# Kernel optimization log

Measured on AMD Instinct MI355X. Metric: run time of the kernel, lower is better.

## Reference

```python
import jax, jax.numpy as jnp
import numpy as np

N, E, F_IN, H, L = 100000, 1600000, 256, 128, 4
ALPHA, THETA, EPS = 0.1, 0.5, 1e-5


def setup_inputs() -> dict:
    key = jax.random.key(0)
    ks = jax.random.split(key, 6)
    x = jax.random.normal(ks[0], (N, F_IN), dtype=jnp.float32)
    edge_index = jax.random.randint(ks[1], (2, E), 0, N, dtype=jnp.int32)
    lin0_w = jax.random.normal(ks[2], (F_IN, H), dtype=jnp.float32) / np.sqrt(F_IN)
    lin0_b = jnp.zeros((H,), dtype=jnp.float32)
    conv_w = jax.random.normal(ks[3], (L, H, H), dtype=jnp.float32) / np.sqrt(H)
    bn_gamma = jnp.ones((L - 1, H), dtype=jnp.float32)
    bn_beta = jnp.zeros((L - 1, H), dtype=jnp.float32)
    return {"x": x, "edge_index": edge_index, "lin0_w": lin0_w, "lin0_b": lin0_b,
            "conv_w": conv_w, "bn_gamma": bn_gamma, "bn_beta": bn_beta}


def reference(x, edge_index, lin0_w, lin0_b, conv_w, bn_gamma, bn_beta):
    n = x.shape[0]
    loops = jnp.arange(n, dtype=edge_index.dtype)
    row = jnp.concatenate([edge_index[0], loops])  # source
    col = jnp.concatenate([edge_index[1], loops])  # target
    # GCN symmetric normalization with self-loops: D^{-1/2}(A+I)D^{-1/2}
    deg = jax.ops.segment_sum(jnp.ones_like(col, dtype=x.dtype), col, num_segments=n)
    dinv = jnp.where(deg > 0, jax.lax.rsqrt(deg), 0.0)
    norm = (dinv[row] * dinv[col])[:, None]  # [E+N, 1]

    def prop(h):  # sparse aggregation: out[c] += norm * h[r]
        return jax.ops.segment_sum(h[row] * norm, col, num_segments=n)

    # GCNConv input layer
    z = prop(x @ lin0_w) + lin0_b
    x0 = z
    for i in range(L):
        h = prop(z)
        beta = float(np.log(THETA / (i + 1) + 1.0))
        s = (1.0 - ALPHA) * h + ALPHA * x0          # identity mapping to initial features
        z = (1.0 - beta) * s + beta * (s @ conv_w[i])  # shared_weights GCN2Conv
        if i < L - 1:
            mu = jnp.mean(z, axis=0)
            var = jnp.mean((z - mu) ** 2, axis=0)
            z = (z - mu) * jax.lax.rsqrt(var + EPS) * bn_gamma[i] + bn_beta[i]
            z = jax.nn.relu(z)
    return z
```

## Files before the change

### kernel.cpp

```cpp
#include <hip/hip_runtime.h>
#include <hip/hip_bf16.h>
#include <math.h>

#define H 128
#define EPS_BN 1e-5f
#define RSTATS 16

typedef __attribute__((ext_vector_type(8))) short short8;
typedef __attribute__((ext_vector_type(4))) float f32x4;

__device__ __forceinline__ float bf2f(ushort u){
  union { float f; uint v; } x; x.v = ((uint)u) << 16; return x.f;
}
__device__ __forceinline__ ushort f2bf(float f){
  union { float f; uint v; } x; x.f = f;
  uint v = x.v;
  uint r = v + 0x7fff + ((v >> 16) & 1);
  return (ushort)(r >> 16);
}

__device__ __forceinline__ void acc8(float* a, uint4 v, float wt){
  a[0] += wt*bf2f((ushort)(v.x & 0xffff)); a[1] += wt*bf2f((ushort)(v.x >> 16));
  a[2] += wt*bf2f((ushort)(v.y & 0xffff)); a[3] += wt*bf2f((ushort)(v.y >> 16));
  a[4] += wt*bf2f((ushort)(v.z & 0xffff)); a[5] += wt*bf2f((ushort)(v.z >> 16));
  a[6] += wt*bf2f((ushort)(v.w & 0xffff)); a[7] += wt*bf2f((ushort)(v.w >> 16));
}


__global__ void k_count(const int* __restrict__ col, int E, int* __restrict__ cnt){
  int i = blockIdx.x*blockDim.x + threadIdx.x;
  if (i < E) atomicAdd(&cnt[col[i]], 1);
}

__global__ void k_dinv(const int* __restrict__ cnt, float* __restrict__ dinv, int n){
  int i = blockIdx.x*blockDim.x + threadIdx.x;
  if (i < n) dinv[i] = rsqrtf((float)cnt[i] + 1.0f);
}

__global__ void k_scan1(const int* __restrict__ cnt, int* __restrict__ off,
                        int* __restrict__ bsum, int n){
  __shared__ int s[1024];
  int t = threadIdx.x;
  int i = blockIdx.x*1024 + t;
  int v = (i < n) ? cnt[i] : 0;
  s[t] = v; __syncthreads();
  for (int d = 1; d < 1024; d <<= 1){
    int x = (t >= d) ? s[t-d] : 0;
    __syncthreads();
    s[t] += x;
    __syncthreads();
  }
  if (i < n) off[i] = s[t] - v;
  if (t == 1023) bsum[blockIdx.x] = s[1023];
}

__global__ void k_scan2(int* bsum, int nb){
  int l = threadIdx.x;
  int carry = 0;
  for (int b0 = 0; b0 < nb; b0 += 64){
    int i = b0 + l;
    int orig = (i < nb) ? bsum[i] : 0;
    int v = orig;
    #pragma unroll
    for (int d = 1; d < 64; d <<= 1){
      int x = __shfl_up(v, d);
      if (l >= d) v += x;
    }
    if (i < nb) bsum[i] = carry + v - orig;
    carry += __shfl(v, 63);
  }
}

__global__ void k_scan3(int* __restrict__ off, int* __restrict__ cursor,
                        const int* __restrict__ bsum, int n, int Etot){
  int i = blockIdx.x*blockDim.x + threadIdx.x;
  if (i < n){ int o = off[i] + bsum[i >> 10]; off[i] = o; cursor[i] = o; }
  if (i == 0) off[n] = Etot;
}

__global__ void k_fill(const int* __restrict__ row, const int* __restrict__ col, int E,
                       const float* __restrict__ dinv, int* __restrict__ cursor,
                       uint2* __restrict__ edge){
  int i = blockIdx.x*blockDim.x + threadIdx.x;
  if (i < E){
    int c = col[i], r = row[i];
    int p = atomicAdd(&cursor[c], 1);
    edge[p] = make_uint2((uint)r, __float_as_uint(dinv[r]*dinv[c]));
  }
}


__global__ void k_prepw(const float* __restrict__ lin0_w, const float* __restrict__ conv_w,
                        ushort* __restrict__ lin0T, ushort* __restrict__ WpT,
                        float b0, float b1, float b2, float b3){
  int i = blockIdx.x*blockDim.x + threadIdx.x;
  if (i < 128*256){
    int nn = i >> 8, k = i & 255;
    lin0T[i] = f2bf(lin0_w[k*128 + nn]);
  } else if (i < 128*256 + 4*128*128){
    int j = i - 128*256;
    int ll = j >> 14, rc = j & 16383;
    int nn = rc >> 7, k = rc & 127;
    float beta = (ll==0)?b0:(ll==1)?b1:(ll==2)?b2:b3;
    float v = beta * conv_w[ll*16384 + k*128 + nn];
    if (k == nn) v += 1.0f - beta;
    WpT[j] = f2bf(v);
  }
}


__device__ __forceinline__ void gather_node(
    float* a, const ushort* __restrict__ zin, const uint2* __restrict__ edge,
    const float* __restrict__ dinv, int node, int e0, int e1, int lr){
  float wc = dinv[node]; wc *= wc;
  uint4 vs = *(const uint4*)(zin + (size_t)node*H + lr*8);
  int e = e0;
  for (; e + 3 < e1; e += 4){
    uint2 er0 = edge[e],   er1 = edge[e+1];
    uint2 er2 = edge[e+2], er3 = edge[e+3];
    uint4 v0 = *(const uint4*)(zin + (size_t)er0.x*H + lr*8);
    uint4 v1 = *(const uint4*)(zin + (size_t)er1.x*H + lr*8);
    uint4 v2 = *(const uint4*)(zin + (size_t)er2.x*H + lr*8);
    uint4 v3 = *(const uint4*)(zin + (size_t)er3.x*H + lr*8);
    acc8(a, v0, __uint_as_float(er0.y));
    acc8(a, v1, __uint_as_float(er1.y));
    acc8(a, v2, __uint_as_float(er2.y));
    acc8(a, v3, __uint_as_float(er3.y));
  }
  for (; e < e1; ++e){
    uint2 er = edge[e];
    uint4 v = *(const uint4*)(zin + (size_t)er.x*H + lr*8);
    acc8(a, v, __uint_as_float(er.y));
  }
  acc8(a, vs, wc);
}


__global__ __launch_bounds__(256) void k_prop0(
    const ushort* __restrict__ h, const int* __restrict__ off,
    const uint2* __restrict__ edge, const float* __restrict__ dinv,
    const float* __restrict__ bias,
    ushort* __restrict__ x0, int n){
  int gq = (blockIdx.x*blockDim.x + threadIdx.x) >> 4;
  if (gq >= n) return;
  int lr = threadIdx.x & 15;
  int e0 = off[gq], e1 = off[gq+1];
  float a[8];
  #pragma unroll
  for (int j = 0; j < 8; ++j) a[j] = 0.f;
  gather_node(a, h, edge, dinv, gq, e0, e1, lr);
  float4 b0 = *(const float4*)(bias + lr*8);
  float4 b1 = *(const float4*)(bias + lr*8 + 4);
  uint4 pk;
  pk.x = (uint)f2bf(a[0]+b0.x) | ((uint)f2bf(a[1]+b0.y) << 16);
  pk.y = (uint)f2bf(a[2]+b0.z) | ((uint)f2bf(a[3]+b0.w) << 16);
  pk.z = (uint)f2bf(a[4]+b1.x) | ((uint)f2bf(a[5]+b1.y) << 16);
  pk.w = (uint)f2bf(a[6]+b1.z) | ((uint)f2bf(a[7]+b1.w) << 16);
  *(uint4*)(x0 + (size_t)gq*H + lr*8) = pk;
}


template<bool STATS, bool OUTF32>
__global__ __launch_bounds__(256) void k_layer(
    const ushort* __restrict__ zin, const ushort* __restrict__ x0,
    const int* __restrict__ off, const uint2* __restrict__ edge,
    const float* __restrict__ dinv, const ushort* __restrict__ BT,
    void* __restrict__ zout, float* __restrict__ stats, int n)
{
  __shared__ ushort Sm[32*128];
  int t = threadIdx.x;
  int w = t >> 6, l = t & 63;
  int lr = l & 15, q = l >> 4;
  int base = blockIdx.x * 32;

  #pragma unroll
  for (int g2 = 0; g2 < 2; ++g2){
    int row  = w*8 + g2*4 + q;
    int node = base + row;
    float a[8];
    #pragma unroll
    for (int j = 0; j < 8; ++j) a[j] = 0.f;
    uint4 pk = make_uint4(0u,0u,0u,0u);
    if (node < n){
      int e0 = off[node], e1 = off[node+1];
      gather_node(a, zin, edge, dinv, node, e0, e1, lr);
      uint4 xv = *(const uint4*)(x0 + (size_t)node*H + lr*8);
      float s0 = 0.9f*a[0] + 0.1f*bf2f((ushort)(xv.x & 0xffff));
      float s1 = 0.9f*a[1] + 0.1f*bf2f((ushort)(xv.x >> 16));
      float s2 = 0.9f*a[2] + 0.1f*bf2f((ushort)(xv.y & 0xffff));
      float s3 = 0.9f*a[3] + 0.1f*bf2f((ushort)(xv.y >> 16));
      float s4 = 0.9f*a[4] + 0.1f*bf2f((ushort)(xv.z & 0xffff));
      float s5 = 0.9f*a[5] + 0.1f*bf2f((ushort)(xv.z >> 16));
      float s6 = 0.9f*a[6] + 0.1f*bf2f((ushort)(xv.w & 0xffff));
      float s7 = 0.9f*a[7] + 0.1f*bf2f((ushort)(xv.w >> 16));
      pk.x = (uint)f2bf(s0) | ((uint)f2bf(s1) << 16);
      pk.y = (uint)f2bf(s2) | ((uint)f2bf(s3) << 16);
      pk.z = (uint)f2bf(s4) | ((uint)f2bf(s5) << 16);
      pk.w = (uint)f2bf(s6) | ((uint)f2bf(s7) << 16);
    }
    *(uint4*)(&Sm[row*128 + ((lr ^ (row & 15))*8)]) = pk;
  }

  short8 bfr[2][4];
  #pragma unroll
  for (int c = 0; c < 2; ++c)
    #pragma unroll
    for (int ks = 0; ks < 4; ++ks)
      bfr[c][ks] = *(const short8*)(BT + (size_t)(w*32 + c*16 + lr)*H + ks*32 + q*8);

  __syncthreads();

  f32x4 acc[2][2];
  #pragma unroll
  for (int rt = 0; rt < 2; ++rt){
    acc[rt][0] = (f32x4){0.f,0.f,0.f,0.f};
    acc[rt][1] = (f32x4){0.f,0.f,0.f,0.f};
  }
  #pragma unroll
  for (int rt = 0; rt < 2; ++rt){
    int row = rt*16 + lr;
    #pragma unroll
    for (int ks = 0; ks < 4; ++ks){
      short8 af = *(const short8*)(&Sm[row*128 + (((ks*4 + q) ^ (row & 15))*8)]);
      acc[rt][0] = __builtin_amdgcn_mfma_f32_16x16x32_bf16(af, bfr[0][ks], acc[rt][0], 0,0,0);
      acc[rt][1] = __builtin_amdgcn_mfma_f32_16x16x32_bf16(af, bfr[1][ks], acc[rt][1], 0,0,0);
    }
  }

  #pragma unroll
  for (int rt = 0; rt < 2; ++rt){
    #pragma unroll
    for (int c = 0; c < 2; ++c){
      #pragma unroll
      for (int j = 0; j < 4; ++j){
        int row = base + rt*16 + q*4 + j;
        float v = acc[rt][c][j];
        if (OUTF32){
          if (row < n)
            ((float*)zout)[(size_t)row*H + w*32 + c*16 + lr] = v;
        } else {
          float other = __shfl(v, l ^ 1);
          if (!(lr & 1) && row < n){
            uint pk = (uint)f2bf(v) | ((uint)f2bf(other) << 16);
            ((uint*)zout)[(size_t)row*64 + w*16 + c*8 + (lr >> 1)] = pk;
          }
        }
      }
    }
  }
  if (STATS){
    #pragma unroll
    for (int c = 0; c < 2; ++c){
      float sv = 0.f, sq = 0.f;
      #pragma unroll
      for (int rt = 0; rt < 2; ++rt)
        #pragma unroll
        for (int j = 0; j < 4; ++j){
          float v = acc[rt][c][j];
          sv += v; sq += v*v;
        }
      sv += __shfl(sv, l ^ 16); sv += __shfl(sv, l ^ 32);
      sq += __shfl(sq, l ^ 16); sq += __shfl(sq, l ^ 32);
      if (q == 0){
        float* st = stats + (size_t)(blockIdx.x & (RSTATS-1))*256;
        atomicAdd(&st[w*32 + c*16 + lr], sv);
        atomicAdd(&st[128 + w*32 + c*16 + lr], sq);
      }
    }
  }
}


__global__ void k_bnfinal(const float* __restrict__ stats, const float* __restrict__ gamma,
                          const float* __restrict__ beta, float* __restrict__ scsh,
                          float inv_n){
  int f = threadIdx.x;
  float s = 0.f, s2 = 0.f;
  for (int r = 0; r < RSTATS; ++r){
    s  += stats[r*256 + f];
    s2 += stats[r*256 + 128 + f];
  }
  float mu  = s * inv_n;
  float var = s2 * inv_n - mu*mu;
  float sc  = rsqrtf(var + EPS_BN) * gamma[f];
  scsh[f]       = sc;
  scsh[128 + f] = beta[f] - mu*sc;
}


__global__ __launch_bounds__(256) void k_bnapply(
    uint4* __restrict__ z, const float* __restrict__ scsh, int n16){
  int i = blockIdx.x*blockDim.x + threadIdx.x;
  if (i >= n16) return;
  int f8 = (i & 15) * 8;
  uint4 v = z[i];
  uint r[4];
  #pragma unroll
  for (int p = 0; p < 4; ++p){
    uint  u  = (&v.x)[p];
    float z0 = bf2f((ushort)(u & 0xffff));
    float z1 = bf2f((ushort)(u >> 16));
    float y0 = fmaxf(fmaf(z0, scsh[f8 + p*2],     scsh[128 + f8 + p*2]),     0.f);
    float y1 = fmaxf(fmaf(z1, scsh[f8 + p*2 + 1], scsh[128 + f8 + p*2 + 1]), 0.f);
    r[p] = (uint)f2bf(y0) | ((uint)f2bf(y1) << 16);
  }
  z[i] = make_uint4(r[0], r[1], r[2], r[3]);
}


__global__ __launch_bounds__(256) void k_gemm0(
    const float* __restrict__ Af, const ushort* __restrict__ BT,
    ushort* __restrict__ Cb, int n){
  const int K = 256;
  __shared__ ushort As[64*32];
  __shared__ ushort Bs[128*32];
  int t = threadIdx.x;
  int br = blockIdx.x * 64;
  int w = t >> 6, l = t & 63;
  int lr = l & 15, lk = l >> 4;
  int swz = (lr >> 1) & 3;

  f32x4 acc[8];
  #pragma unroll
  for (int i = 0; i < 8; ++i) acc[i] = (f32x4){0.f,0.f,0.f,0.f};

  int sar = t >> 2;
  int sab = t & 3;
  int sa_off = sar*32 + ((sab ^ ((sar>>1)&3))*8);

  for (int k0 = 0; k0 < K; k0 += 32){
    int grow = br + sar;
    float4 v0 = make_float4(0.f,0.f,0.f,0.f), v1 = v0;
    if (grow < n){
      v0 = *(const float4*)(Af + (size_t)grow*K + k0 + sab*8);
      v1 = *(const float4*)(Af + (size_t)grow*K + k0 + sab*8 + 4);
    }
    ushort tmp[8] = {f2bf(v0.x),f2bf(v0.y),f2bf(v0.z),f2bf(v0.w),
                     f2bf(v1.x),f2bf(v1.y),f2bf(v1.z),f2bf(v1.w)};
    *(uint4*)(&As[sa_off]) = *(const uint4*)tmp;
    #pragma unroll
    for (int i = 0; i < 2; ++i){
      int qq = t + i*256;
      int nrow = qq >> 2, bb = qq & 3;
      uint4 v = *(const uint4*)(BT + (size_t)nrow*K + k0 + bb*8);
      *(uint4*)(&Bs[nrow*32 + ((bb ^ ((nrow>>1)&3))*8)]) = v;
    }
    __syncthreads();
    short8 af = *(const short8*)(&As[(w*16+lr)*32 + ((lk ^ swz)*8)]);
    #pragma unroll
    for (int tn = 0; tn < 8; ++tn){
      short8 bfv = *(const short8*)(&Bs[(tn*16+lr)*32 + ((lk ^ swz)*8)]);
      acc[tn] = __builtin_amdgcn_mfma_f32_16x16x32_bf16(af, bfv, acc[tn], 0, 0, 0);
    }
    __syncthreads();
  }
  int orow = br + w*16 + lk*4;
  #pragma unroll
  for (int tn = 0; tn < 8; ++tn){
    #pragma unroll
    for (int j = 0; j < 4; ++j){
      float mine  = acc[tn][j];
      float other = __shfl(mine, l ^ 1);
      if (!(l & 1) && (orow + j) < n){
        uint pk = (uint)f2bf(mine) | ((uint)f2bf(other) << 16);
        ((uint*)Cb)[(size_t)(orow+j)*64 + tn*8 + (lr >> 1)] = pk;
      }
    }
  }
}


extern "C" void kernel_launch(void* const* d_in, const int* in_sizes, int n_in,
                              void* d_out, int out_size, void* d_ws, size_t ws_size,
                              hipStream_t stream){
  const float* x        = (const float*)d_in[0];
  const int*   ei       = (const int*)  d_in[1];
  const float* lin0_w   = (const float*)d_in[2];
  const float* lin0_b   = (const float*)d_in[3];
  const float* conv_w   = (const float*)d_in[4];
  const float* bn_gamma = (const float*)d_in[5];
  const float* bn_beta  = (const float*)d_in[6];
  float* out = (float*)d_out;

  int N = in_sizes[0] / 256;
  int E = in_sizes[1] / 2;
  const int* row = ei;
  const int* col = ei + E;

  char* ws = (char*)d_ws;
  size_t p = 0;
  auto alloc = [&](size_t bytes)->char*{
    char* r = ws + p; p = (p + bytes + 255) & ~(size_t)255; return r;
  };
  int*    cnt    = (int*)   alloc((size_t)N*4);
  int*    off    = (int*)   alloc((size_t)(N+1)*4);
  int*    cursor = (int*)   alloc((size_t)N*4);
  float*  dinv   = (float*) alloc((size_t)N*4);
  int*    bsum   = (int*)   alloc(512*4);
  uint2*  edge   = (uint2*) alloc((size_t)E*8);
  ushort* zb     = (ushort*)alloc((size_t)N*H*2);
  ushort* sb     = (ushort*)alloc((size_t)N*H*2);
  ushort* x0b    = (ushort*)alloc((size_t)N*H*2);
  ushort* lin0T  = (ushort*)alloc(128*256*2);
  ushort* WpT    = (ushort*)alloc(4*128*128*2);
  float*  stats  = (float*) alloc(RSTATS*256*4);
  float*  scsh   = (float*) alloc(2*128*4);

  float betas[4];
  for (int i = 0; i < 4; ++i) betas[i] = logf(0.5f/(float)(i+1) + 1.0f);
  float inv_n = 1.0f/(float)N;

  hipMemsetAsync(cnt, 0, (size_t)N*4, stream);
  k_count<<<(E+255)/256, 256, 0, stream>>>(col, E, cnt);
  k_dinv <<<(N+255)/256, 256, 0, stream>>>(cnt, dinv, N);
  int nb = (N + 1023)/1024;
  k_scan1<<<nb, 1024, 0, stream>>>(cnt, off, bsum, N);
  k_scan2<<<1, 64, 0, stream>>>(bsum, nb);
  k_scan3<<<(N+255)/256, 256, 0, stream>>>(off, cursor, bsum, N, E);
  k_fill <<<(E+255)/256, 256, 0, stream>>>(row, col, E, dinv, cursor, edge);

  k_prepw<<<(128*256 + 4*128*128 + 255)/256, 256, 0, stream>>>(
      lin0_w, conv_w, lin0T, WpT, betas[0], betas[1], betas[2], betas[3]);

  int gemm_blocks = (N + 63)/64;
  int lay_blocks  = (N + 31)/32;
  int prop_blocks = (N + 15)/16;
  int bn_blocks   = ((N*16) + 255)/256;

  k_gemm0<<<gemm_blocks, 256, 0, stream>>>(x, lin0T, sb, N);
  k_prop0<<<prop_blocks, 256, 0, stream>>>(sb, off, edge, dinv, lin0_b, x0b, N);

  hipMemsetAsync(stats, 0, RSTATS*256*4, stream);
  k_layer<true,false><<<lay_blocks, 256, 0, stream>>>(
      x0b, x0b, off, edge, dinv, WpT + 0*128*128, sb, stats, N);
  k_bnfinal<<<1, 128, 0, stream>>>(stats, bn_gamma + 0*H, bn_beta + 0*H, scsh, inv_n);
  k_bnapply<<<bn_blocks, 256, 0, stream>>>((uint4*)sb, scsh, N*16);

  hipMemsetAsync(stats, 0, RSTATS*256*4, stream);
  k_layer<true,false><<<lay_blocks, 256, 0, stream>>>(
      sb, x0b, off, edge, dinv, WpT + 1*128*128, zb, stats, N);
  k_bnfinal<<<1, 128, 0, stream>>>(stats, bn_gamma + 1*H, bn_beta + 1*H, scsh, inv_n);
  k_bnapply<<<bn_blocks, 256, 0, stream>>>((uint4*)zb, scsh, N*16);

  hipMemsetAsync(stats, 0, RSTATS*256*4, stream);
  k_layer<true,false><<<lay_blocks, 256, 0, stream>>>(
      zb, x0b, off, edge, dinv, WpT + 2*128*128, sb, stats, N);
  k_bnfinal<<<1, 128, 0, stream>>>(stats, bn_gamma + 2*H, bn_beta + 2*H, scsh, inv_n);
  k_bnapply<<<bn_blocks, 256, 0, stream>>>((uint4*)sb, scsh, N*16);

  k_layer<false,true><<<lay_blocks, 256, 0, stream>>>(
      sb, x0b, off, edge, dinv, WpT + 3*128*128, out, nullptr, N);
}
```

Before: 613.1 us.

## Build CSR via two-pass counting sort so neighbor lists are source-ordered

Replaces the single atomic scatter into target-CSR with a two-pass counting sort: edges are first bucketed by source, then scattered by target. Within each target row the neighbors end up roughly sorted by source index, which should improve locality of the gathers in every propagation pass. It also folds the dinv computation into the scan kernel and zeroes the BN stats inside k_bnfinal, removing a kernel and several memsets. The cost is extra preprocessing: a second histogram, scan and scatter pass that reuses the zb buffer as temporary storage.

```diff
diff --git a/kernel.cpp b/kernel.cpp
--- a/kernel.cpp
+++ b/kernel.cpp
@@ -27,22 +27,22 @@
 }
 
 
-__global__ void k_count(const int* __restrict__ col, int E, int* __restrict__ cnt){
-  int i = blockIdx.x*blockDim.x + threadIdx.x;
-  if (i < E) atomicAdd(&cnt[col[i]], 1);
-}
-
-__global__ void k_dinv(const int* __restrict__ cnt, float* __restrict__ dinv, int n){
-  int i = blockIdx.x*blockDim.x + threadIdx.x;
-  if (i < n) dinv[i] = rsqrtf((float)cnt[i] + 1.0f);
+__global__ void k_count2(const int* __restrict__ row, const int* __restrict__ col,
+                         int E, int* __restrict__ cnt_t, int* __restrict__ cnt_s){
+  int i = blockIdx.x*blockDim.x + threadIdx.x;
+  if (i < E){
+    atomicAdd(&cnt_t[col[i]], 1);
+    atomicAdd(&cnt_s[row[i]], 1);
+  }
 }
 
 __global__ void k_scan1(const int* __restrict__ cnt, int* __restrict__ off,
-                        int* __restrict__ bsum, int n){
+                        int* __restrict__ bsum, float* __restrict__ dinv, int n){
   __shared__ int s[1024];
   int t = threadIdx.x;
   int i = blockIdx.x*1024 + t;
   int v = (i < n) ? cnt[i] : 0;
+  if (dinv && i < n) dinv[i] = rsqrtf((float)v + 1.0f);
   s[t] = v; __syncthreads();
   for (int d = 1; d < 1024; d <<= 1){
     int x = (t >= d) ? s[t-d] : 0;
@@ -78,13 +78,24 @@
   if (i == 0) off[n] = Etot;
 }
 
-__global__ void k_fill(const int* __restrict__ row, const int* __restrict__ col, int E,
-                       const float* __restrict__ dinv, int* __restrict__ cursor,
-                       uint2* __restrict__ edge){
+__global__ void k_fillA(const int* __restrict__ row, const int* __restrict__ col, int E,
+                        int* __restrict__ cur_s, uint2* __restrict__ tmp){
   int i = blockIdx.x*blockDim.x + threadIdx.x;
   if (i < E){
-    int c = col[i], r = row[i];
-    int p = atomicAdd(&cursor[c], 1);
+    int r = row[i], c = col[i];
+    int p = atomicAdd(&cur_s[r], 1);
+    tmp[p] = make_uint2((uint)r, (uint)c);
+  }
+}
+
+__global__ void k_fillB(const uint2* __restrict__ tmp, int E,
+                        const float* __restrict__ dinv, int* __restrict__ cur_t,
+                        uint2* __restrict__ edge){
+  int i = blockIdx.x*blockDim.x + threadIdx.x;
+  if (i < E){
+    uint2 rc = tmp[i];
+    int r = (int)rc.x, c = (int)rc.y;
+    int p = atomicAdd(&cur_t[c], 1);
     edge[p] = make_uint2((uint)r, __float_as_uint(dinv[r]*dinv[c]));
   }
 }
@@ -271,7 +282,7 @@
 }
 
 
-__global__ void k_bnfinal(const float* __restrict__ stats, const float* __restrict__ gamma,
+__global__ void k_bnfinal(float* __restrict__ stats, const float* __restrict__ gamma,
                           const float* __restrict__ beta, float* __restrict__ scsh,
                           float inv_n){
   int f = threadIdx.x;
@@ -279,6 +290,8 @@
   for (int r = 0; r < RSTATS; ++r){
     s  += stats[r*256 + f];
     s2 += stats[r*256 + 128 + f];
+    stats[r*256 + f] = 0.f;
+    stats[r*256 + 128 + f] = 0.f;
   }
   float mu  = s * inv_n;
   float var = s2 * inv_n - mu*mu;
@@ -392,9 +405,12 @@
   auto alloc = [&](size_t bytes)->char*{
     char* r = ws + p; p = (p + bytes + 255) & ~(size_t)255; return r;
   };
-  int*    cnt    = (int*)   alloc((size_t)N*4);
-  int*    off    = (int*)   alloc((size_t)(N+1)*4);
-  int*    cursor = (int*)   alloc((size_t)N*4);
+  int*    cnt_t  = (int*)   alloc((size_t)N*4);
+  int*    off_t  = (int*)   alloc((size_t)(N+1)*4);
+  int*    cur_t  = (int*)   alloc((size_t)N*4);
+  int*    cnt_s  = (int*)   alloc((size_t)N*4);
+  int*    off_s  = (int*)   alloc((size_t)(N+1)*4);
+  int*    cur_s  = (int*)   alloc((size_t)N*4);
   float*  dinv   = (float*) alloc((size_t)N*4);
   int*    bsum   = (int*)   alloc(512*4);
   uint2*  edge   = (uint2*) alloc((size_t)E*8);
@@ -406,18 +422,24 @@
   float*  stats  = (float*) alloc(RSTATS*256*4);
   float*  scsh   = (float*) alloc(2*128*4);
 
+  uint2* tmp = (uint2*)zb;
+
   float betas[4];
   for (int i = 0; i < 4; ++i) betas[i] = logf(0.5f/(float)(i+1) + 1.0f);
   float inv_n = 1.0f/(float)N;
 
-  hipMemsetAsync(cnt, 0, (size_t)N*4, stream);
-  k_count<<<(E+255)/256, 256, 0, stream>>>(col, E, cnt);
-  k_dinv <<<(N+255)/256, 256, 0, stream>>>(cnt, dinv, N);
+  hipMemsetAsync(cnt_t, 0, (size_t)N*4, stream);
+  hipMemsetAsync(cnt_s, 0, (size_t)N*4, stream);
+  k_count2<<<(E+255)/256, 256, 0, stream>>>(row, col, E, cnt_t, cnt_s);
   int nb = (N + 1023)/1024;
-  k_scan1<<<nb, 1024, 0, stream>>>(cnt, off, bsum, N);
+  k_scan1<<<nb, 1024, 0, stream>>>(cnt_t, off_t, bsum, dinv, N);
   k_scan2<<<1, 64, 0, stream>>>(bsum, nb);
-  k_scan3<<<(N+255)/256, 256, 0, stream>>>(off, cursor, bsum, N, E);
-  k_fill <<<(E+255)/256, 256, 0, stream>>>(row, col, E, dinv, cursor, edge);
+  k_scan3<<<(N+255)/256, 256, 0, stream>>>(off_t, cur_t, bsum, N, E);
+  k_scan1<<<nb, 1024, 0, stream>>>(cnt_s, off_s, bsum, nullptr, N);
+  k_scan2<<<1, 64, 0, stream>>>(bsum, nb);
+  k_scan3<<<(N+255)/256, 256, 0, stream>>>(off_s, cur_s, bsum, N, E);
+  k_fillA<<<(E+255)/256, 256, 0, stream>>>(row, col, E, cur_s, tmp);
+  k_fillB<<<(E+255)/256, 256, 0, stream>>>(tmp, E, dinv, cur_t, edge);
 
   k_prepw<<<(128*256 + 4*128*128 + 255)/256, 256, 0, stream>>>(
       lin0_w, conv_w, lin0T, WpT, betas[0], betas[1], betas[2], betas[3]);
@@ -428,26 +450,25 @@
   int bn_blocks   = ((N*16) + 255)/256;
 
   k_gemm0<<<gemm_blocks, 256, 0, stream>>>(x, lin0T, sb, N);
-  k_prop0<<<prop_blocks, 256, 0, stream>>>(sb, off, edge, dinv, lin0_b, x0b, N);
+  k_prop0<<<prop_blocks, 256, 0, stream>>>(sb, off_t, edge, dinv, lin0_b, x0b, N);
 
   hipMemsetAsync(stats, 0, RSTATS*256*4, stream);
+
   k_layer<true,false><<<lay_blocks, 256, 0, stream>>>(
-      x0b, x0b, off, edge, dinv, WpT + 0*128*128, sb, stats, N);
+      x0b, x0b, off_t, edge, dinv, WpT + 0*128*128, sb, stats, N);
   k_bnfinal<<<1, 128, 0, stream>>>(stats, bn_gamma + 0*H, bn_beta + 0*H, scsh, inv_n);
   k_bnapply<<<bn_blocks, 256, 0, stream>>>((uint4*)sb, scsh, N*16);
 
-  hipMemsetAsync(stats, 0, RSTATS*256*4, stream);
   k_layer<true,false><<<lay_blocks, 256, 0, stream>>>(
-      sb, x0b, off, edge, dinv, WpT + 1*128*128, zb, stats, N);
+      sb, x0b, off_t, edge, dinv, WpT + 1*128*128, zb, stats, N);
   k_bnfinal<<<1, 128, 0, stream>>>(stats, bn_gamma + 1*H, bn_beta + 1*H, scsh, inv_n);
   k_bnapply<<<bn_blocks, 256, 0, stream>>>((uint4*)zb, scsh, N*16);
 
-  hipMemsetAsync(stats, 0, RSTATS*256*4, stream);
   k_layer<true,false><<<lay_blocks, 256, 0, stream>>>(
-      zb, x0b, off, edge, dinv, WpT + 2*128*128, sb, stats, N);
+      zb, x0b, off_t, edge, dinv, WpT + 2*128*128, sb, stats, N);
   k_bnfinal<<<1, 128, 0, stream>>>(stats, bn_gamma + 2*H, bn_beta + 2*H, scsh, inv_n);
   k_bnapply<<<bn_blocks, 256, 0, stream>>>((uint4*)sb, scsh, N*16);
 
   k_layer<false,true><<<lay_blocks, 256, 0, stream>>>(
-      sb, x0b, off, edge, dinv, WpT + 3*128*128, out, nullptr, N);
-}
+      sb, x0b, off_t, edge, dinv, WpT + 3*128*128, out, nullptr, N);
+}
```

New measurement: 801.5 us. 30.7% more time.

## Reorder layer nodes by degree to balance per-wavefront gather work

Applied to the files above, without the earlier changes.

Builds a degree-sorted node permutation with a histogram, scan and scatter, and the fused layer kernel processes nodes in that order, so rows sharing a block have similar edge counts and wavefronts diverge less. It also folds the dinv computation into the first scan kernel, moves the stats reset into k_bnfinal to drop memsets, and reuses the self-row load as x0 in the first layer. In exchange it adds three small setup kernels and scattered output writes that lose contiguous row locality.

```diff
diff --git a/kernel.cpp b/kernel.cpp
--- a/kernel.cpp
+++ b/kernel.cpp
@@ -32,17 +32,13 @@
   if (i < E) atomicAdd(&cnt[col[i]], 1);
 }
 
-__global__ void k_dinv(const int* __restrict__ cnt, float* __restrict__ dinv, int n){
-  int i = blockIdx.x*blockDim.x + threadIdx.x;
-  if (i < n) dinv[i] = rsqrtf((float)cnt[i] + 1.0f);
-}
-
 __global__ void k_scan1(const int* __restrict__ cnt, int* __restrict__ off,
-                        int* __restrict__ bsum, int n){
+                        int* __restrict__ bsum, float* __restrict__ dinv, int n){
   __shared__ int s[1024];
   int t = threadIdx.x;
   int i = blockIdx.x*1024 + t;
   int v = (i < n) ? cnt[i] : 0;
+  if (i < n) dinv[i] = rsqrtf((float)v + 1.0f);
   s[t] = v; __syncthreads();
   for (int d = 1; d < 1024; d <<= 1){
     int x = (t >= d) ? s[t-d] : 0;
@@ -86,6 +82,39 @@
     int c = col[i], r = row[i];
     int p = atomicAdd(&cursor[c], 1);
     edge[p] = make_uint2((uint)r, __float_as_uint(dinv[r]*dinv[c]));
+  }
+}
+
+
+__global__ void k_dhist(const int* __restrict__ cnt, int* __restrict__ dh, int n){
+  int i = blockIdx.x*blockDim.x + threadIdx.x;
+  if (i < n){
+    int d = cnt[i]; if (d > 255) d = 255;
+    atomicAdd(&dh[d], 1);
+  }
+}
+
+__global__ void k_dscan(int* __restrict__ dh){
+  __shared__ int s[256];
+  int t = threadIdx.x;
+  int v = dh[t];
+  s[t] = v; __syncthreads();
+  for (int d = 1; d < 256; d <<= 1){
+    int x = (t >= d) ? s[t-d] : 0;
+    __syncthreads();
+    s[t] += x;
+    __syncthreads();
+  }
+  dh[t] = s[t] - v;
+}
+
+__global__ void k_dperm(const int* __restrict__ cnt, int* __restrict__ dh,
+                        int* __restrict__ perm, int n){
+  int i = blockIdx.x*blockDim.x + threadIdx.x;
+  if (i < n){
+    int d = cnt[i]; if (d > 255) d = 255;
+    int p = atomicAdd(&dh[d], 1);
+    perm[p] = i;
   }
 }
 
@@ -109,11 +138,9 @@
 }
 
 
-__device__ __forceinline__ void gather_node(
+__device__ __forceinline__ void gather_edges(
     float* a, const ushort* __restrict__ zin, const uint2* __restrict__ edge,
-    const float* __restrict__ dinv, int node, int e0, int e1, int lr){
-  float wc = dinv[node]; wc *= wc;
-  uint4 vs = *(const uint4*)(zin + (size_t)node*H + lr*8);
+    int e0, int e1, int lr){
   int e = e0;
   for (; e + 3 < e1; e += 4){
     uint2 er0 = edge[e],   er1 = edge[e+1];
@@ -132,7 +159,6 @@
     uint4 v = *(const uint4*)(zin + (size_t)er.x*H + lr*8);
     acc8(a, v, __uint_as_float(er.y));
   }
-  acc8(a, vs, wc);
 }
 
 
@@ -144,11 +170,13 @@
   int gq = (blockIdx.x*blockDim.x + threadIdx.x) >> 4;
   if (gq >= n) return;
   int lr = threadIdx.x & 15;
-  int e0 = off[gq], e1 = off[gq+1];
   float a[8];
   #pragma unroll
   for (int j = 0; j < 8; ++j) a[j] = 0.f;
-  gather_node(a, h, edge, dinv, gq, e0, e1, lr);
+  float wc = dinv[gq]; wc *= wc;
+  uint4 vs = *(const uint4*)(h + (size_t)gq*H + lr*8);
+  gather_edges(a, h, edge, off[gq], off[gq+1], lr);
+  acc8(a, vs, wc);
   float4 b0 = *(const float4*)(bias + lr*8);
   float4 b1 = *(const float4*)(bias + lr*8 + 4);
   uint4 pk;
@@ -160,31 +188,37 @@
 }
 
 
-template<bool STATS, bool OUTF32>
+template<bool STATS, bool OUTF32, bool SAMEX0>
 __global__ __launch_bounds__(256) void k_layer(
     const ushort* __restrict__ zin, const ushort* __restrict__ x0,
     const int* __restrict__ off, const uint2* __restrict__ edge,
     const float* __restrict__ dinv, const ushort* __restrict__ BT,
+    const int* __restrict__ perm,
     void* __restrict__ zout, float* __restrict__ stats, int n)
 {
   __shared__ ushort Sm[32*128];
+  __shared__ int pm[32];
   int t = threadIdx.x;
   int w = t >> 6, l = t & 63;
   int lr = l & 15, q = l >> 4;
   int base = blockIdx.x * 32;
+  if (t < 32) pm[t] = (base + t < n) ? perm[base + t] : -1;
+  __syncthreads();
 
   #pragma unroll
   for (int g2 = 0; g2 < 2; ++g2){
     int row  = w*8 + g2*4 + q;
-    int node = base + row;
+    int node = pm[row];
     float a[8];
     #pragma unroll
     for (int j = 0; j < 8; ++j) a[j] = 0.f;
     uint4 pk = make_uint4(0u,0u,0u,0u);
-    if (node < n){
-      int e0 = off[node], e1 = off[node+1];
-      gather_node(a, zin, edge, dinv, node, e0, e1, lr);
-      uint4 xv = *(const uint4*)(x0 + (size_t)node*H + lr*8);
+    if (node >= 0){
+      float wc = dinv[node]; wc *= wc;
+      uint4 vs = *(const uint4*)(zin + (size_t)node*H + lr*8);
+      gather_edges(a, zin, edge, off[node], off[node+1], lr);
+      acc8(a, vs, wc);
+      uint4 xv = SAMEX0 ? vs : *(const uint4*)(x0 + (size_t)node*H + lr*8);
       float s0 = 0.9f*a[0] + 0.1f*bf2f((ushort)(xv.x & 0xffff));
       float s1 = 0.9f*a[1] + 0.1f*bf2f((ushort)(xv.x >> 16));
       float s2 = 0.9f*a[2] + 0.1f*bf2f((ushort)(xv.y & 0xffff));
@@ -232,17 +266,18 @@
     #pragma unroll
     for (int c = 0; c < 2; ++c){
       #pragma unroll
-      for (int j = 0; j < 4; ++j){
-        int row = base + rt*16 + q*4 + j;
-        float v = acc[rt][c][j];
+      for (int j2 = 0; j2 < 4; ++j2){
+        int rowl = rt*16 + q*4 + j2;
+        int nodeo = pm[rowl];
+        float v = acc[rt][c][j2];
         if (OUTF32){
-          if (row < n)
-            ((float*)zout)[(size_t)row*H + w*32 + c*16 + lr] = v;
+          if (nodeo >= 0)
+            ((float*)zout)[(size_t)nodeo*H + w*32 + c*16 + lr] = v;
         } else {
           float other = __shfl(v, l ^ 1);
-          if (!(lr & 1) && row < n){
+          if (!(lr & 1) && nodeo >= 0){
             uint pk = (uint)f2bf(v) | ((uint)f2bf(other) << 16);
-            ((uint*)zout)[(size_t)row*64 + w*16 + c*8 + (lr >> 1)] = pk;
+            ((uint*)zout)[(size_t)nodeo*64 + w*16 + c*8 + (lr >> 1)] = pk;
           }
         }
       }
@@ -255,8 +290,8 @@
       #pragma unroll
       for (int rt = 0; rt < 2; ++rt)
         #pragma unroll
-        for (int j = 0; j < 4; ++j){
-          float v = acc[rt][c][j];
+        for (int j2 = 0; j2 < 4; ++j2){
+          float v = acc[rt][c][j2];
           sv += v; sq += v*v;
         }
       sv += __shfl(sv, l ^ 16); sv += __shfl(sv, l ^ 32);
@@ -271,7 +306,7 @@
 }
 
 
-__global__ void k_bnfinal(const float* __restrict__ stats, const float* __restrict__ gamma,
+__global__ void k_bnfinal(float* __restrict__ stats, const float* __restrict__ gamma,
                           const float* __restrict__ beta, float* __restrict__ scsh,
                           float inv_n){
   int f = threadIdx.x;
@@ -279,6 +314,8 @@
   for (int r = 0; r < RSTATS; ++r){
     s  += stats[r*256 + f];
     s2 += stats[r*256 + 128 + f];
+    stats[r*256 + f] = 0.f;
+    stats[r*256 + 128 + f] = 0.f;
   }
   float mu  = s * inv_n;
   float var = s2 * inv_n - mu*mu;
@@ -397,6 +434,8 @@
   int*    cursor = (int*)   alloc((size_t)N*4);
   float*  dinv   = (float*) alloc((size_t)N*4);
   int*    bsum   = (int*)   alloc(512*4);
+  int*    dh     = (int*)   alloc(256*4);
+  int*    perm   = (int*)   alloc((size_t)N*4);
   uint2*  edge   = (uint2*) alloc((size_t)E*8);
   ushort* zb     = (ushort*)alloc((size_t)N*H*2);
   ushort* sb     = (ushort*)alloc((size_t)N*H*2);
@@ -411,10 +450,13 @@
   float inv_n = 1.0f/(float)N;
 
   hipMemsetAsync(cnt, 0, (size_t)N*4, stream);
+  hipMemsetAsync(dh, 0, 256*4, stream);
   k_count<<<(E+255)/256, 256, 0, stream>>>(col, E, cnt);
-  k_dinv <<<(N+255)/256, 256, 0, stream>>>(cnt, dinv, N);
+  k_dhist<<<(N+255)/256, 256, 0, stream>>>(cnt, dh, N);
+  k_dscan<<<1, 256, 0, stream>>>(dh);
+  k_dperm<<<(N+255)/256, 256, 0, stream>>>(cnt, dh, perm, N);
   int nb = (N + 1023)/1024;
-  k_scan1<<<nb, 1024, 0, stream>>>(cnt, off, bsum, N);
+  k_scan1<<<nb, 1024, 0, stream>>>(cnt, off, bsum, dinv, N);
   k_scan2<<<1, 64, 0, stream>>>(bsum, nb);
   k_scan3<<<(N+255)/256, 256, 0, stream>>>(off, cursor, bsum, N, E);
   k_fill <<<(E+255)/256, 256, 0, stream>>>(row, col, E, dinv, cursor, edge);
@@ -431,23 +473,22 @@
   k_prop0<<<prop_blocks, 256, 0, stream>>>(sb, off, edge, dinv, lin0_b, x0b, N);
 
   hipMemsetAsync(stats, 0, RSTATS*256*4, stream);
-  k_layer<true,false><<<lay_blocks, 256, 0, stream>>>(
-      x0b, x0b, off, edge, dinv, WpT + 0*128*128, sb, stats, N);
+
+  k_layer<true,false,true><<<lay_blocks, 256, 0, stream>>>(
+      x0b, x0b, off, edge, dinv, WpT + 0*128*128, perm, sb, stats, N);
   k_bnfinal<<<1, 128, 0, stream>>>(stats, bn_gamma + 0*H, bn_beta + 0*H, scsh, inv_n);
   k_bnapply<<<bn_blocks, 256, 0, stream>>>((uint4*)sb, scsh, N*16);
 
-  hipMemsetAsync(stats, 0, RSTATS*256*4, stream);
-  k_layer<true,false><<<lay_blocks, 256, 0, stream>>>(
-      sb, x0b, off, edge, dinv, WpT + 1*128*128, zb, stats, N);
+  k_layer<true,false,false><<<lay_blocks, 256, 0, stream>>>(
+      sb, x0b, off, edge, dinv, WpT + 1*128*128, perm, zb, stats, N);
   k_bnfinal<<<1, 128, 0, stream>>>(stats, bn_gamma + 1*H, bn_beta + 1*H, scsh, inv_n);
   k_bnapply<<<bn_blocks, 256, 0, stream>>>((uint4*)zb, scsh, N*16);
 
-  hipMemsetAsync(stats, 0, RSTATS*256*4, stream);
-  k_layer<true,false><<<lay_blocks, 256, 0, stream>>>(
-      zb, x0b, off, edge, dinv, WpT + 2*128*128, sb, stats, N);
+  k_layer<true,false,false><<<lay_blocks, 256, 0, stream>>>(
+      zb, x0b, off, edge, dinv, WpT + 2*128*128, perm, sb, stats, N);
   k_bnfinal<<<1, 128, 0, stream>>>(stats, bn_gamma + 2*H, bn_beta + 2*H, scsh, inv_n);
   k_bnapply<<<bn_blocks, 256, 0, stream>>>((uint4*)sb, scsh, N*16);
 
-  k_layer<false,true><<<lay_blocks, 256, 0, stream>>>(
-      sb, x0b, off, edge, dinv, WpT + 3*128*128, out, nullptr, N);
-}
+  k_layer<false,true,false><<<lay_blocks, 256, 0, stream>>>(
+      sb, x0b, off, edge, dinv, WpT + 3*128*128, perm, out, nullptr, N);
+}
```

Measured after the change: 1.103 ms. 1.8x slower.
